# Optimization experiments

Measured on AMD Instinct MI355X. Metric: run time of the kernel, lower is better.

## Reference

```python
import jax, jax.numpy as jnp
import numpy as np

TOPK = 100  # hardcoded in Block: kNNAttention(..., topk=100)
EPS = 1e-5  # torch LayerNorm default


def layer_norm(x, w, b):
    m = jnp.mean(x, axis=-1, keepdims=True)
    v = jnp.mean(jnp.square(x - m), axis=-1, keepdims=True)
    return (x - m) * jax.lax.rsqrt(v + EPS) * w + b


def setup_inputs() -> dict:
    key = jax.random.key(0)
    ks = jax.random.split(key, 8)
    B, N, C, H = 32, 512, 768, 12
    hid = 4 * C
    s_in = 1.0 / np.sqrt(C)
    s_hid = 1.0 / np.sqrt(hid)
    return {
        "x": jax.random.normal(ks[0], (B, N, C), jnp.float32),
        "islast": 0,
        "ln1_w": jnp.ones((C,), jnp.float32),
        "ln1_b": jnp.zeros((C,), jnp.float32),
        "qkv_w": jax.random.normal(ks[1], (3 * C, C), jnp.float32) * s_in,  # qkv_bias=False
        "proj_w": jax.random.normal(ks[2], (C, C), jnp.float32) * s_in,
        "proj_b": jnp.zeros((C,), jnp.float32),
        "ln2_w": jnp.ones((C,), jnp.float32),
        "ln2_b": jnp.zeros((C,), jnp.float32),
        "fc1_w": jax.random.normal(ks[3], (hid, C), jnp.float32) * s_in,
        "fc1_b": jnp.zeros((hid,), jnp.float32),
        "fc2_w": jax.random.normal(ks[4], (C, hid), jnp.float32) * s_hid,
        "fc2_b": jnp.zeros((C,), jnp.float32),
    }


def reference(x, islast, ln1_w, ln1_b, qkv_w, proj_w, proj_b, ln2_w, ln2_b, fc1_w, fc1_b, fc2_w, fc2_b):
    B, N, C = x.shape
    H = 12
    D = C // H
    scale = D ** -0.5

    # --- kNN attention on norm1(x) ---
    xn = layer_norm(x, ln1_w, ln1_b)
    qkv = (xn @ qkv_w.T).reshape(B, N, 3, H, D)
    q, k, v = (qkv[:, :, 0].transpose(0, 2, 1, 3),
               qkv[:, :, 1].transpose(0, 2, 1, 3),
               qkv[:, :, 2].transpose(0, 2, 1, 3))  # [B,H,N,D]
    attn = jnp.einsum("bhnd,bhmd->bhnm", q, k) * scale  # [B,H,N,N]
    if not bool(islast):
        # top-k mask per query row (equivalent to topk + scatter mask; ties measure-zero for floats)
        kth = jax.lax.top_k(attn, TOPK)[0][..., -1:]
        attn = jnp.where(attn >= kth, attn, -jnp.inf)
    attn = jax.nn.softmax(attn, axis=-1)
    out = jnp.einsum("bhnm,bhmd->bhnd", attn, v).transpose(0, 2, 1, 3).reshape(B, N, C)
    out = out @ proj_w.T + proj_b
    x = x + out  # residual (drop_path/dropout = 0, eval)

    # --- MLP on norm2(x) ---
    xn2 = layer_norm(x, ln2_w, ln2_b)
    h = jax.nn.gelu(xn2 @ fc1_w.T + fc1_b, approximate=False)
    x = x + (h @ fc2_w.T + fc2_b)
    return x, attn
```

## Files before the change

kernel.cpp:

```cpp
#include <hip/hip_runtime.h>
#include <hip/hip_bf16.h>
#include <math.h>

using bf16 = __hip_bfloat16;
typedef __attribute__((ext_vector_type(8))) short bh8;
typedef __attribute__((ext_vector_type(4))) float f4;

static const long long X_ELEMS = 12582912LL;

enum { EPI_F32 = 0, EPI_BIAS_RES = 2, EPI_BIAS_GELU = 3, EPI_QKV = 4, EPI_PV = 5 };

__device__ __forceinline__ float fin(float v) {
  return (fabsf(v) < 1e30f) ? v : 0.f;
}
__device__ __forceinline__ unsigned short f2bf(float f) {
  bf16 h = __float2bfloat16(f);
  return *reinterpret_cast<unsigned short*>(&h);
}
__device__ __forceinline__ uint4 pack8(float4 a, float4 b) {
  union { uint4 u; unsigned short h[8]; } r;
  r.h[0] = f2bf(a.x); r.h[1] = f2bf(a.y); r.h[2] = f2bf(a.z); r.h[3] = f2bf(a.w);
  r.h[4] = f2bf(b.x); r.h[5] = f2bf(b.y); r.h[6] = f2bf(b.z); r.h[7] = f2bf(b.w);
  return r.u;
}
__device__ __forceinline__ void gl_lds16(const bf16* g, unsigned short* l) {
  __builtin_amdgcn_global_load_lds((const __attribute__((address_space(1))) void*)g,
                                   (__attribute__((address_space(3))) void*)l, 16, 0, 0);
}

__global__ __launch_bounds__(256) void cast_all(const float* __restrict__ qkv_w,
    const float* __restrict__ proj_w, const float* __restrict__ fc1_w,
    const float* __restrict__ fc2_w, bf16* __restrict__ dst) {
  int i = blockIdx.x * 256 + threadIdx.x;
  const float* s; int base;
  if (i < 442368)       { s = qkv_w;  base = 0; }
  else if (i < 589824)  { s = proj_w; base = 442368; }
  else if (i < 1179648) { s = fc1_w;  base = 589824; }
  else                  { s = fc2_w;  base = 1179648; }
  float4 f = ((const float4*)s)[i - base];
  union { uint2 u; unsigned short h[4]; } r;
  r.h[0] = f2bf(f.x); r.h[1] = f2bf(f.y); r.h[2] = f2bf(f.z); r.h[3] = f2bf(f.w);
  ((uint2*)dst)[i] = r.u;
}

__global__ __launch_bounds__(256) void ln_kernel(const float* __restrict__ x,
    const float* __restrict__ w, const float* __restrict__ bi, bf16* __restrict__ out) {
  int row = blockIdx.x; int t = threadIdx.x;
  const float* xr = x + (size_t)row * 768;
  float v0 = xr[t], v1 = xr[t + 256], v2 = xr[t + 512];
  float s = v0 + v1 + v2;
  float s2 = v0 * v0 + v1 * v1 + v2 * v2;
  for (int off = 32; off; off >>= 1) { s += __shfl_down(s, off); s2 += __shfl_down(s2, off); }
  __shared__ float ls[4], ls2[4];
  int wid = t >> 6, lane = t & 63;
  if (lane == 0) { ls[wid] = s; ls2[wid] = s2; }
  __syncthreads();
  float S = ls[0] + ls[1] + ls[2] + ls[3];
  float S2 = ls2[0] + ls2[1] + ls2[2] + ls2[3];
  float mean = S * (1.0f / 768.0f);
  float var = S2 * (1.0f / 768.0f) - mean * mean;
  float rstd = rsqrtf(fmaxf(var, 0.f) + 1e-5f);
  bf16* orow = out + (size_t)row * 768;
  orow[t]       = __float2bfloat16((v0 - mean) * rstd * w[t]       + bi[t]);
  orow[t + 256] = __float2bfloat16((v1 - mean) * rstd * w[t + 256] + bi[t + 256]);
  orow[t + 512] = __float2bfloat16((v2 - mean) * rstd * w[t + 512] + bi[t + 512]);
}

template<int BN, int EPI, bool AF32>
__global__ __launch_bounds__(256)
void gemm_bt(const void* __restrict__ A, const bf16* __restrict__ B, void* __restrict__ Cout,
             int M, int N, int K,
             long long sA, long long sB, long long sC,
             const float* __restrict__ bias, const float* __restrict__ resid, float alpha,
             bf16* __restrict__ qo, bf16* __restrict__ ko, bf16* __restrict__ vo) {
  const int BM = 128, BK = 32;
  const int WN = BN / 2;
  const int NB = WN / 16;
  __shared__ unsigned short As[BM * BK];
  __shared__ unsigned short Bs[BN * BK];
  int t = threadIdx.x;
  int wid = t >> 6, lane = t & 63;
  int wm = wid >> 1, wn = wid & 1;
  int m0 = blockIdx.y * BM;
  int n0 = blockIdx.x * BN;
  int z = blockIdx.z;

  f4 acc[4][NB];
#pragma unroll
  for (int i = 0; i < 4; i++)
#pragma unroll
    for (int j = 0; j < NB; j++) acc[i][j] = f4{0.f, 0.f, 0.f, 0.f};

  int rowT = t >> 2;
  int colT = (t & 3) * 8;
  int q16 = lane >> 4;
  int r16 = lane & 15;

  unsigned short* lA = As + (size_t)wid * 512;
  unsigned short* lB = Bs + (size_t)wid * 512;

  for (int k0 = 0; k0 < K; k0 += BK) {
    uint4 a0, a1;
    if (AF32) {
      const float* aP = (const float*)A + (long long)z * sA + (long long)(m0 + rowT) * K + (k0 + colT);
      float4 f0 = *(const float4*)aP, f1 = *(const float4*)(aP + 4);
      a0 = pack8(f0, f1);
      const float* aQ = aP + (long long)64 * K;
      f0 = *(const float4*)aQ; f1 = *(const float4*)(aQ + 4);
      a1 = pack8(f0, f1);
    }
    __syncthreads();
    if (AF32) {
      *(uint4*)&As[rowT * BK + colT] = a0;
      *(uint4*)&As[(rowT + 64) * BK + colT] = a1;
    } else {
      const bf16* aP = (const bf16*)A + (long long)z * sA + (long long)(m0 + rowT) * K + (k0 + colT);
      gl_lds16(aP, lA);
      gl_lds16(aP + (long long)64 * K, lA + 2048);
    }
    {
      const bf16* bP = B + (long long)z * sB + (long long)(n0 + rowT) * K + (k0 + colT);
      gl_lds16(bP, lB);
      if (BN == 128) gl_lds16(bP + (long long)64 * K, lB + 2048);
    }
    asm volatile("s_waitcnt vmcnt(0)" ::: "memory");
    __syncthreads();

    bh8 af[4], bfr[NB];
#pragma unroll
    for (int i = 0; i < 4; i++) {
      int r = wm * 64 + i * 16 + r16;
      af[i] = *(const bh8*)&As[r * BK + q16 * 8];
    }
#pragma unroll
    for (int j = 0; j < NB; j++) {
      int r = wn * WN + j * 16 + r16;
      bfr[j] = *(const bh8*)&Bs[r * BK + q16 * 8];
    }
#pragma unroll
    for (int i = 0; i < 4; i++)
#pragma unroll
      for (int j = 0; j < NB; j++)
        acc[i][j] = __builtin_amdgcn_mfma_f32_16x16x32_bf16(af[i], bfr[j], acc[i][j], 0, 0, 0);
  }

  long long cbase = (long long)z * sC;
#pragma unroll
  for (int i = 0; i < 4; i++) {
#pragma unroll
    for (int j = 0; j < NB; j++) {
#pragma unroll
      for (int r = 0; r < 4; r++) {
        int mg = m0 + wm * 64 + i * 16 + q16 * 4 + r;
        int ng = n0 + wn * WN + j * 16 + r16;
        float v = acc[i][j][r] * alpha;
        if (EPI == EPI_F32) {
          ((float*)Cout)[cbase + (long long)mg * N + ng] = fin(v);
        } else if (EPI == EPI_BIAS_RES) {
          long long idx = cbase + (long long)mg * N + ng;
          v += bias[ng] + resid[idx];
          ((float*)Cout)[idx] = fin(v);
        } else if (EPI == EPI_BIAS_GELU) {
          v = fin(v + bias[ng]);
          float g = 0.5f * v * (1.0f + erff(v * 0.70710678118654752f));
          ((bf16*)Cout)[cbase + (long long)mg * N + ng] = __float2bfloat16(g);
        } else if (EPI == EPI_QKV) {
          int b = mg >> 9, n = mg & 511;
          int which = ng / 768;
          int c = ng - which * 768;
          int h = c >> 6, d = c & 63;
          size_t zz = (size_t)(b * 12 + h);
          bf16 val = __float2bfloat16(fin(v));
          if (which == 0)      qo[zz * 32768 + n * 64 + d] = val;
          else if (which == 1) ko[zz * 32768 + n * 64 + d] = val;
          else                 vo[(zz * 64 + d) * 512 + n] = val;
        } else {
          int b = z / 12, h = z - b * 12;
          ((bf16*)Cout)[((size_t)(b * 512 + mg)) * 768 + h * 64 + ng] = __float2bfloat16(fin(v));
        }
      }
    }
  }
}

__global__ __launch_bounds__(256)
void attn_topk(const bf16* __restrict__ q, const bf16* __restrict__ kk,
               float* __restrict__ probs, const int* __restrict__ islast) {
  const int SSTR = 516;
  __shared__ float S[16 * SSTR];
  int t = threadIdx.x;
  int wid = t >> 6, lane = t & 63;
  int q16 = lane >> 4, r16 = lane & 15;
  int g = blockIdx.x;
  int xcd = g & 7, idx = g >> 3;
  int z = xcd * 48 + (idx >> 5);
  int qb = idx & 31;
  long long zoff = (long long)z * 32768;

  const bf16* qp = q + zoff + (long long)(qb * 16 + r16) * 64 + q16 * 8;
  union { uint4 u; bh8 h; } uq0, uq1;
  uq0.u = *(const uint4*)qp;
  uq1.u = *(const uint4*)(qp + 32);

  for (int nb = 0; nb < 8; ++nb) {
    int r = wid * 128 + nb * 16 + r16;
    const bf16* kp = kk + zoff + (long long)r * 64 + q16 * 8;
    union { uint4 u; bh8 h; } uk0, uk1;
    uk0.u = *(const uint4*)kp;
    uk1.u = *(const uint4*)(kp + 32);
    f4 a = f4{0.f, 0.f, 0.f, 0.f};
    a = __builtin_amdgcn_mfma_f32_16x16x32_bf16(uq0.h, uk0.h, a, 0, 0, 0);
    a = __builtin_amdgcn_mfma_f32_16x16x32_bf16(uq1.h, uk1.h, a, 0, 0, 0);
    int srow = q16 * 4;
    int scol = wid * 128 + nb * 16 + r16;
#pragma unroll
    for (int rr = 0; rr < 4; ++rr)
      S[(srow + rr) * SSTR + scol] = fin(a[rr] * 0.125f);
  }
  __syncthreads();

  int isl = *islast;
  for (int rp = 0; rp < 4; ++rp) {
    int lrow = wid * 4 + rp;
    const float* sr = S + lrow * SSTR;
    float4 va = ((const float4*)sr)[lane];
    float4 vb = ((const float4*)sr)[lane + 64];
    float v[8] = {va.x, va.y, va.z, va.w, vb.x, vb.y, vb.z, vb.w};
    unsigned key[8];
    float m = -1e30f;
#pragma unroll
    for (int e = 0; e < 8; e++) {
      if (!(v[e] >= -1e38f)) v[e] = -1e38f;
      unsigned u = __float_as_uint(v[e]);
      key[e] = (u & 0x80000000u) ? ~u : (u | 0x80000000u);
      m = fmaxf(m, v[e]);
    }
    for (int off = 32; off; off >>= 1) m = fmaxf(m, __shfl_xor(m, off));

    unsigned T = 0;
    if (isl == 0) {
      for (int bit = 31; bit >= 0; --bit) {
        unsigned Tc = T | (1u << bit);
        int cnt = 0;
#pragma unroll
        for (int e = 0; e < 8; e++) cnt += __popcll(__ballot(key[e] >= Tc));
        if (cnt >= 100) T = Tc;
        if (cnt == 100) break;
      }
    }
    float p[8]; float Z = 0.f;
#pragma unroll
    for (int e = 0; e < 8; e++) { p[e] = (key[e] >= T) ? __expf(v[e] - m) : 0.f; Z += p[e]; }
    for (int off = 32; off; off >>= 1) Z += __shfl_xor(Z, off);
    float rz = (Z > 0.f) ? (1.0f / Z) : 0.f;
    float* og = probs + (long long)z * 262144 + (long long)(qb * 16 + lrow) * 512;
    ((float4*)og)[lane]      = float4{p[0] * rz, p[1] * rz, p[2] * rz, p[3] * rz};
    ((float4*)og)[lane + 64] = float4{p[4] * rz, p[5] * rz, p[6] * rz, p[7] * rz};
  }
}

extern "C" void kernel_launch(void* const* d_in, const int* in_sizes, int n_in,
                              void* d_out, int out_size, void* d_ws, size_t ws_size,
                              hipStream_t stream) {
  const float* x      = (const float*)d_in[0];
  const int*   islast = (const int*)d_in[1];
  const float* ln1_w  = (const float*)d_in[2];
  const float* ln1_b  = (const float*)d_in[3];
  const float* qkv_w  = (const float*)d_in[4];
  const float* proj_w = (const float*)d_in[5];
  const float* proj_b = (const float*)d_in[6];
  const float* ln2_w  = (const float*)d_in[7];
  const float* ln2_b  = (const float*)d_in[8];
  const float* fc1_w  = (const float*)d_in[9];
  const float* fc1_b  = (const float*)d_in[10];
  const float* fc2_w  = (const float*)d_in[11];
  const float* fc2_b  = (const float*)d_in[12];

  char* ws = (char*)d_ws;
  bf16*  wqkv = (bf16*)(ws + 0LL);
  bf16*  wproj= (bf16*)(ws + 3538944LL);
  bf16*  wfc1 = (bf16*)(ws + 4718592LL);
  bf16*  wfc2 = (bf16*)(ws + 9437184LL);
  bf16*  q    = (bf16*)(ws + 14155776LL);
  bf16*  kk   = (bf16*)(ws + 39321600LL);
  bf16*  vT   = (bf16*)(ws + 64487424LL);
  bf16*  AO   = q;
  bf16*  Hbuf = q;
  float* X1   = (float*)(ws + 39321600LL);

  float* outX    = (float*)d_out;
  float* outAttn = outX + X_ELEMS;
  bf16*  XN  = (bf16*)outX;
  bf16*  XN2 = (bf16*)((char*)d_out + 25165824LL);

  cast_all<<<6912, 256, 0, stream>>>(qkv_w, proj_w, fc1_w, fc2_w, wqkv);
  ln_kernel<<<16384, 256, 0, stream>>>(x, ln1_w, ln1_b, XN);
  gemm_bt<128, EPI_QKV, false><<<dim3(18, 128, 1), 256, 0, stream>>>(
      XN, wqkv, nullptr, 16384, 2304, 768, 0, 0, 0, nullptr, nullptr, 1.0f, q, kk, vT);
  attn_topk<<<12288, 256, 0, stream>>>(q, kk, outAttn, islast);
  gemm_bt<64, EPI_PV, true><<<dim3(1, 4, 384), 256, 0, stream>>>(
      outAttn, vT, AO, 512, 64, 512, 262144, 32768, 0, nullptr, nullptr, 1.0f,
      nullptr, nullptr, nullptr);
  gemm_bt<128, EPI_BIAS_RES, false><<<dim3(6, 128, 1), 256, 0, stream>>>(
      AO, wproj, X1, 16384, 768, 768, 0, 0, 0, proj_b, x, 1.0f, nullptr, nullptr, nullptr);
  ln_kernel<<<16384, 256, 0, stream>>>(X1, ln2_w, ln2_b, XN2);
  for (int i = 0; i < 4; ++i) {
    const bf16* xn2c = XN2 + (long long)i * 4096 * 768;
    gemm_bt<128, EPI_BIAS_GELU, false><<<dim3(24, 32, 1), 256, 0, stream>>>(
        xn2c, wfc1, Hbuf, 4096, 3072, 768, 0, 0, 0, fc1_b, nullptr, 1.0f,
        nullptr, nullptr, nullptr);
    gemm_bt<128, EPI_BIAS_RES, false><<<dim3(6, 32, 1), 256, 0, stream>>>(
        Hbuf, wfc2, outX + (long long)i * 4096 * 768, 4096, 768, 3072, 0, 0, 0,
        fc2_b, X1 + (long long)i * 4096 * 768, 1.0f, nullptr, nullptr, nullptr);
  }
  (void)in_sizes; (void)n_in; (void)out_size; (void)ws_size;
}
```

Baseline: 1.409 ms.

## Fuse P·V product into top-k attention kernel and retile fc2 GEMM

The attention kernel now stages the normalized probabilities as bf16 in shared memory and computes the 16-row P·V product with MFMA directly. It writes the head output into a buffer aliased onto the output tensor. This removes the separate PV GEMM launch, which re-read the full fp32 probability matrix from global memory. The fc2 GEMM also switches to a 64-wide tile with twice as many blocks. In exchange, the attention kernel reuses its score shared memory and gains a sync plus extra V loads per block.

```diff
diff --git a/kernel.cpp b/kernel.cpp
--- a/kernel.cpp
+++ b/kernel.cpp
@@ -185,9 +185,11 @@
 
 __global__ __launch_bounds__(256)
 void attn_topk(const bf16* __restrict__ q, const bf16* __restrict__ kk,
-               float* __restrict__ probs, const int* __restrict__ islast) {
+               const bf16* __restrict__ vT, float* __restrict__ probs,
+               bf16* __restrict__ AO, const int* __restrict__ islast) {
   const int SSTR = 516;
   __shared__ float S[16 * SSTR];
+  unsigned short* Pb = (unsigned short*)S;
   int t = threadIdx.x;
   int wid = t >> 6, lane = t & 63;
   int q16 = lane >> 4, r16 = lane & 15;
@@ -256,6 +258,28 @@
     float* og = probs + (long long)z * 262144 + (long long)(qb * 16 + lrow) * 512;
     ((float4*)og)[lane]      = float4{p[0] * rz, p[1] * rz, p[2] * rz, p[3] * rz};
     ((float4*)og)[lane + 64] = float4{p[4] * rz, p[5] * rz, p[6] * rz, p[7] * rz};
+    union { uint2 u; unsigned short h[4]; } pw0, pw1;
+#pragma unroll
+    for (int e = 0; e < 4; e++) { pw0.h[e] = f2bf(p[e] * rz); pw1.h[e] = f2bf(p[4 + e] * rz); }
+    *(uint2*)&Pb[lrow * 1032 + lane * 4]       = pw0.u;
+    *(uint2*)&Pb[lrow * 1032 + 256 + lane * 4] = pw1.u;
+  }
+  __syncthreads();
+
+  int d = wid * 16 + r16;
+  const bf16* vp = vT + zoff + (long long)d * 512 + q16 * 8;
+  f4 acc2 = f4{0.f, 0.f, 0.f, 0.f};
+  for (int kc = 0; kc < 16; ++kc) {
+    bh8 pa = *(const bh8*)&Pb[r16 * 1032 + kc * 32 + q16 * 8];
+    union { uint4 u; bh8 h; } uv;
+    uv.u = *(const uint4*)(vp + kc * 32);
+    acc2 = __builtin_amdgcn_mfma_f32_16x16x32_bf16(pa, uv.h, acc2, 0, 0, 0);
+  }
+  int b = z / 12, h = z - b * 12;
+#pragma unroll
+  for (int rr = 0; rr < 4; ++rr) {
+    int qrow = qb * 16 + q16 * 4 + rr;
+    AO[((size_t)(b * 512 + qrow)) * 768 + h * 64 + d] = __float2bfloat16(fin(acc2[rr]));
   }
 }
 
@@ -284,23 +308,20 @@
   bf16*  q    = (bf16*)(ws + 14155776LL);
   bf16*  kk   = (bf16*)(ws + 39321600LL);
   bf16*  vT   = (bf16*)(ws + 64487424LL);
-  bf16*  AO   = q;
   bf16*  Hbuf = q;
   float* X1   = (float*)(ws + 39321600LL);
 
   float* outX    = (float*)d_out;
   float* outAttn = outX + X_ELEMS;
   bf16*  XN  = (bf16*)outX;
+  bf16*  AO  = (bf16*)outX;
   bf16*  XN2 = (bf16*)((char*)d_out + 25165824LL);
 
   cast_all<<<6912, 256, 0, stream>>>(qkv_w, proj_w, fc1_w, fc2_w, wqkv);
   ln_kernel<<<16384, 256, 0, stream>>>(x, ln1_w, ln1_b, XN);
   gemm_bt<128, EPI_QKV, false><<<dim3(18, 128, 1), 256, 0, stream>>>(
       XN, wqkv, nullptr, 16384, 2304, 768, 0, 0, 0, nullptr, nullptr, 1.0f, q, kk, vT);
-  attn_topk<<<12288, 256, 0, stream>>>(q, kk, outAttn, islast);
-  gemm_bt<64, EPI_PV, true><<<dim3(1, 4, 384), 256, 0, stream>>>(
-      outAttn, vT, AO, 512, 64, 512, 262144, 32768, 0, nullptr, nullptr, 1.0f,
-      nullptr, nullptr, nullptr);
+  attn_topk<<<12288, 256, 0, stream>>>(q, kk, vT, outAttn, AO, islast);
   gemm_bt<128, EPI_BIAS_RES, false><<<dim3(6, 128, 1), 256, 0, stream>>>(
       AO, wproj, X1, 16384, 768, 768, 0, 0, 0, proj_b, x, 1.0f, nullptr, nullptr, nullptr);
   ln_kernel<<<16384, 256, 0, stream>>>(X1, ln2_w, ln2_b, XN2);
@@ -309,7 +330,7 @@
     gemm_bt<128, EPI_BIAS_GELU, false><<<dim3(24, 32, 1), 256, 0, stream>>>(
         xn2c, wfc1, Hbuf, 4096, 3072, 768, 0, 0, 0, fc1_b, nullptr, 1.0f,
         nullptr, nullptr, nullptr);
-    gemm_bt<128, EPI_BIAS_RES, false><<<dim3(6, 32, 1), 256, 0, stream>>>(
+    gemm_bt<64, EPI_BIAS_RES, false><<<dim3(12, 32, 1), 256, 0, stream>>>(
         Hbuf, wfc2, outX + (long long)i * 4096 * 768, 4096, 768, 3072, 0, 0, 0,
         fc2_b, X1 + (long long)i * 4096 * 768, 1.0f, nullptr, nullptr, nullptr);
   }
```

New measurement: 1.316 ms. 1.07x faster.
